# Kernel optimization log

Measured on AMD Instinct MI355X. Metric: run time of the kernel, lower is better.

The kernel has to match this reference:

```python
import jax, jax.numpy as jnp
import numpy as np

N_NODES = 50000
N_EDGES = 800000
IN_F, OUT_F = 128, 128
NUM_HEADS, QUERY_DIM = 3, 8


def setup_inputs() -> dict:
    key = jax.random.key(0)
    ks = jax.random.split(key, 8)
    scale = 1.0 / np.sqrt(IN_F)
    return {
        "x": jax.random.normal(ks[0], (N_NODES, IN_F), dtype=jnp.float32),
        "adj": jax.random.randint(ks[1], (2, N_EDGES), 0, N_NODES, dtype=jnp.int64),
        "Wq": jax.random.normal(ks[2], (QUERY_DIM * NUM_HEADS, IN_F), dtype=jnp.float32) * scale,
        "bq": jax.random.normal(ks[3], (QUERY_DIM * NUM_HEADS,), dtype=jnp.float32) * 0.01,
        "aw": jax.random.normal(ks[4], (NUM_HEADS, 2 * QUERY_DIM * NUM_HEADS), dtype=jnp.float32) * 0.1,
        "ab": jax.random.normal(ks[5], (NUM_HEADS,), dtype=jnp.float32) * 0.01,
        "lw": jax.random.normal(ks[6], (OUT_F, IN_F), dtype=jnp.float32) * scale,
        "lb": jax.random.normal(ks[7], (OUT_F,), dtype=jnp.float32) * 0.01,
    }


def reference(x, adj, Wq, bq, aw, ab, lw, lb):
    n = x.shape[0]
    s, r = adj[0], adj[1]
    # per-node query features: [N, H*Q]
    attr = x @ Wq.T + bq
    # per-edge attention logits from concat(sender, receiver): [E, H]
    e = jnp.concatenate((attr[s], attr[r]), axis=1) @ aw.T + ab
    # segment softmax over incoming edges of each receiver
    seg_max = jax.ops.segment_max(e, r, num_segments=n)  # [N, H]
    e = jnp.exp(e - jax.lax.stop_gradient(seg_max)[r])
    denom = jax.ops.segment_sum(e, r, num_segments=n)  # [N, H]
    alpha = e / jnp.maximum(denom[r], 1e-16)  # [E, H]
    # node value projection and attention-weighted aggregation
    h = x @ lw.T + lb  # [N, OUT_F]
    msg = h[s] * alpha.mean(axis=1, keepdims=True)  # [E, OUT_F]
    out = jax.ops.segment_sum(msg, r, num_segments=n)  # [N, OUT_F]
    return jax.nn.silu(out)
```

## Files before the change

kernel.cpp:

```cpp
#include <hip/hip_runtime.h>
#include <hip/hip_fp16.h>
#include <math.h>

#define N_NODES 50000
#define N_EDGES 800000
#define IN_F 128
#define OUT_F 128
#define NH 3
#define SCAN_NB ((N_NODES + 255) / 256)
#define NODE_NB ((N_NODES + 31) / 32)
#define NBH 32
#define EPB (N_EDGES / NBH)
#define QNODES (N_NODES / 4)
#define CQ_BLOCKS (NBH * 4)
#define NSLICE 4
#define SLICE_HALVES ((size_t)N_NODES * 32)

typedef __attribute__((ext_vector_type(8))) _Float16 f16x8;
typedef __attribute__((ext_vector_type(4))) float f32x4;
typedef __attribute__((ext_vector_type(2))) int i32x2;

__global__ __launch_bounds__(256) void weights_kernel(
    const float* __restrict__ Wq, const float* __restrict__ bq,
    const float* __restrict__ aw, const float* __restrict__ ab,
    const float* __restrict__ lw,
    _Float16* __restrict__ w2h, float* __restrict__ b2,
    _Float16* __restrict__ lwh)
{
    int t = blockIdx.x * 256 + threadIdx.x;
    if (t < 16 * 128) {
        int prow = t >> 7;
        int i    = t & 127;
        int r = -1;
        if (prow < 3) r = prow;
        else if (prow >= 4 && prow < 7) r = prow - 1;
        if (r < 0) {
            w2h[prow * 128 + i] = (_Float16)0.0f;
        } else {
            int hh  = (r < 3) ? r : r - 3;
            int off = (r < 3) ? 0 : 24;
            const float* awr = aw + hh * 48 + off;
            float acc = 0.0f;
            #pragma unroll
            for (int q = 0; q < 24; q++) acc += awr[q] * Wq[q * 128 + i];
            w2h[prow * 128 + i] = (_Float16)acc;
            if (i == 0) {
                float b = 0.0f;
                #pragma unroll
                for (int q = 0; q < 24; q++) b += awr[q] * bq[q];
                if (r >= 3) b += ab[hh];
                b2[r] = b;
            }
        }
    }
    int u = t - 16 * 128;
    if (u >= 0 && u < 128 * 128) lwh[u] = (_Float16)lw[u];
}

__global__ __launch_bounds__(256) void node_count_kernel(
    const float* __restrict__ x, const _Float16* __restrict__ lwh,
    const float* __restrict__ lb, const _Float16* __restrict__ w2h,
    const float* __restrict__ b2, const int* __restrict__ adj,
    __half* __restrict__ h, float* __restrict__ as4, float* __restrict__ ar4,
    unsigned int* __restrict__ hist, unsigned short* __restrict__ rank)
{
    __shared__ __align__(16) unsigned int shmem[QNODES / 2];

    if (blockIdx.x < CQ_BLOCKS) {
        unsigned int* cnt = shmem;
        for (int i = threadIdx.x; i < QNODES / 2; i += 256) cnt[i] = 0;
        __syncthreads();
        const int c = blockIdx.x >> 2, q = blockIdx.x & 3;
        const int nlo = q * QNODES;
        const int e0 = c * EPB, e1 = e0 + EPB;
        for (int base = e0 + threadIdx.x; base < e1; base += 8 * 256) {
            int rs[8];
            #pragma unroll
            for (int u = 0; u < 8; u++) {
                int e = base + u * 256;
                rs[u] = (e < e1) ? adj[N_EDGES + e] : -1;
            }
            #pragma unroll
            for (int u = 0; u < 8; u++) {
                int e = base + u * 256;
                int lr = rs[u] - nlo;
                if ((unsigned)lr < (unsigned)QNODES) {
                    int sh = (lr & 1) * 16;
                    unsigned int old = atomicAdd(&cnt[lr >> 1], 1u << sh);
                    rank[e] = (unsigned short)(old >> sh);
                }
            }
        }
        __syncthreads();
        unsigned int* hb = hist + (size_t)c * (N_NODES / 2) + q * (QNODES / 2);
        for (int i = threadIdx.x; i < QNODES / 2; i += 256)
            hb[i] = cnt[i];
        return;
    }

    unsigned char* xs = (unsigned char*)shmem;
    const int tx = threadIdx.x;
    const int nb = (blockIdx.x - CQ_BLOCKS) * 32;

    #pragma unroll
    for (int it = 0; it < 2; it++) {
        int cc = it * 256 + tx;
        int node = cc >> 4, kc = cc & 15;
        int gn = nb + node;
        f16x8 v;
        if (gn < N_NODES) {
            const float4* xr = (const float4*)(x + (size_t)gn * 128 + kc * 8);
            float4 p = xr[0], qq = xr[1];
            v[0] = (_Float16)p.x;  v[1] = (_Float16)p.y;
            v[2] = (_Float16)p.z;  v[3] = (_Float16)p.w;
            v[4] = (_Float16)qq.x; v[5] = (_Float16)qq.y;
            v[6] = (_Float16)qq.z; v[7] = (_Float16)qq.w;
        } else {
            #pragma unroll
            for (int e = 0; e < 8; e++) v[e] = (_Float16)0.0f;
        }
        int byte = node * 256 + ((kc * 16) ^ ((node & 7) << 4));
        *(f16x8*)(xs + byte) = v;
    }
    __syncthreads();

    const int wave = tx >> 6, lane = tx & 63;
    const int l15 = lane & 15, lg = lane >> 4;

    f16x8 afr[2][4];
    #pragma unroll
    for (int m = 0; m < 2; m++) {
        int out = wave * 32 + m * 16 + l15;
        const f16x8* ar8 = (const f16x8*)(lwh + (size_t)out * 128);
        #pragma unroll
        for (int kk = 0; kk < 4; kk++)
            afr[m][kk] = ar8[kk * 4 + lg];
    }
    f16x8 a6[4];
    {
        const f16x8* w8 = (const f16x8*)(w2h + (size_t)l15 * 128);
        #pragma unroll
        for (int kk = 0; kk < 4; kk++) a6[kk] = w8[kk * 4 + lg];
    }

    f32x4 acc[2][2], acc6[2];
    #pragma unroll
    for (int m = 0; m < 2; m++)
        #pragma unroll
        for (int n = 0; n < 2; n++)
            acc[m][n] = (f32x4){0.f, 0.f, 0.f, 0.f};
    #pragma unroll
    for (int n = 0; n < 2; n++) acc6[n] = (f32x4){0.f, 0.f, 0.f, 0.f};

    #pragma unroll
    for (int kk = 0; kk < 4; kk++) {
        f16x8 bfr[2];
        #pragma unroll
        for (int n = 0; n < 2; n++) {
            int node = n * 16 + l15;
            int byte = node * 256 + ((kk * 64 + lg * 16) ^ ((node & 7) << 4));
            bfr[n] = *(const f16x8*)(xs + byte);
        }
        #pragma unroll
        for (int m = 0; m < 2; m++)
            #pragma unroll
            for (int n = 0; n < 2; n++)
                acc[m][n] = __builtin_amdgcn_mfma_f32_16x16x32_f16(
                    afr[m][kk], bfr[n], acc[m][n], 0, 0, 0);
        if (wave == 0) {
            #pragma unroll
            for (int n = 0; n < 2; n++)
                acc6[n] = __builtin_amdgcn_mfma_f32_16x16x32_f16(
                    a6[kk], bfr[n], acc6[n], 0, 0, 0);
        }
    }

    #pragma unroll
    for (int n = 0; n < 2; n++) {
        int gn = nb + n * 16 + l15;
        if (gn >= N_NODES) continue;
        #pragma unroll
        for (int m = 0; m < 2; m++) {
            int outb = wave * 32 + m * 16 + lg * 4;
            float4 lbv = *(const float4*)&lb[outb];
            __half2 p0 = __floats2half2_rn(acc[m][n].x + lbv.x, acc[m][n].y + lbv.y);
            __half2 p1 = __floats2half2_rn(acc[m][n].z + lbv.z, acc[m][n].w + lbv.w);
            int2 st;
            st.x = *(int*)&p0;
            st.y = *(int*)&p1;
            *(int2*)&h[(size_t)wave * SLICE_HALVES + (size_t)gn * 32 + (outb & 31)] = st;
        }
    }

    if (wave == 0 && lg < 2) {
        float b0, bx, by;
        if (lg == 0) { b0 = b2[0]; bx = b2[1]; by = b2[2]; }
        else         { b0 = b2[3]; bx = b2[4]; by = b2[5]; }
        #pragma unroll
        for (int n = 0; n < 2; n++) {
            int gn = nb + n * 16 + l15;
            if (gn >= N_NODES) continue;
            float4 v = make_float4(acc6[n].x + b0, acc6[n].y + bx,
                                   acc6[n].z + by, 0.0f);
            if (lg == 0) *(float4*)&as4[(size_t)gn * 4] = v;
            else         *(float4*)&ar4[(size_t)gn * 4] = v;
        }
    }
}

__global__ __launch_bounds__(256) void scan_kernel(
    const unsigned int* __restrict__ hist, int* __restrict__ start,
    unsigned short* __restrict__ offs16,
    int* __restrict__ psum, int* __restrict__ poffs, int* __restrict__ sync)
{
    const int t = threadIdx.x, b = blockIdx.x;
    const int i = b * 256 + t;
    const int w = i >> 1, sh = (i & 1) * 16;
    int tot = 0;
    if (i < N_NODES) {
        for (int c = 0; c < NBH; c++)
            tot += (hist[(size_t)c * (N_NODES / 2) + w] >> sh) & 0xffff;
    }
    __shared__ int shm[256];
    shm[t] = tot;
    __syncthreads();
    #pragma unroll
    for (int off = 1; off < 256; off <<= 1) {
        int u = (t >= off) ? shm[t - off] : 0;
        __syncthreads();
        shm[t] += u;
        __syncthreads();
    }
    const int incl = shm[t];
    if (t == 255)
        __hip_atomic_store(&psum[b], incl, __ATOMIC_RELAXED,
                           __HIP_MEMORY_SCOPE_AGENT);
    __syncthreads();
    if (t == 0)
        __hip_atomic_fetch_add(&sync[0], 1, __ATOMIC_RELEASE,
                               __HIP_MEMORY_SCOPE_AGENT);

    if (b == 0) {
        if (t == 0)
            while (__hip_atomic_load(&sync[0], __ATOMIC_ACQUIRE,
                                     __HIP_MEMORY_SCOPE_AGENT) < SCAN_NB) {}
        __syncthreads();
        int pv = (t < SCAN_NB)
               ? __hip_atomic_load(&psum[t], __ATOMIC_RELAXED,
                                   __HIP_MEMORY_SCOPE_AGENT)
               : 0;
        shm[t] = pv;
        __syncthreads();
        #pragma unroll
        for (int off = 1; off < 256; off <<= 1) {
            int u = (t >= off) ? shm[t - off] : 0;
            __syncthreads();
            shm[t] += u;
            __syncthreads();
        }
        if (t < SCAN_NB)
            __hip_atomic_store(&poffs[t], shm[t] - pv, __ATOMIC_RELAXED,
                               __HIP_MEMORY_SCOPE_AGENT);
        __syncthreads();
        if (t == 0)
            __hip_atomic_store(&sync[1], 1, __ATOMIC_RELEASE,
                               __HIP_MEMORY_SCOPE_AGENT);
    }

    if (t == 0)
        while (__hip_atomic_load(&sync[1], __ATOMIC_ACQUIRE,
                                 __HIP_MEMORY_SCOPE_AGENT) == 0) {}
    __syncthreads();
    const int base = __hip_atomic_load(&poffs[b], __ATOMIC_RELAXED,
                                       __HIP_MEMORY_SCOPE_AGENT);
    if (i < N_NODES) {
        start[i] = base + incl - tot;
        int acc = 0;
        for (int c = 0; c < NBH; c++) {
            offs16[(size_t)c * N_NODES + i] = (unsigned short)acc;
            acc += (hist[(size_t)c * (N_NODES / 2) + w] >> sh) & 0xffff;
        }
    }
    if (i == N_NODES - 1) start[N_NODES] = base + incl;
}

__global__ __launch_bounds__(256) void fill_kernel(
    const int* __restrict__ adj, const int* __restrict__ start,
    const unsigned short* __restrict__ offs16,
    const unsigned short* __restrict__ rank,
    unsigned short* __restrict__ srcs)
{
    int e = blockIdx.x * 512 + threadIdx.x;
    #pragma unroll
    for (int u = 0; u < 2; u++, e += 256) {
        if (e < N_EDGES) {
            int r = adj[N_EDGES + e];
            int cb = e / EPB;
            int pos = start[r] + (int)offs16[(size_t)cb * N_NODES + r]
                    + (int)rank[e];
            srcs[pos] = (unsigned short)adj[e];
        }
    }
}

__global__ __launch_bounds__(256) void coef_kernel(
    const int* __restrict__ start, const unsigned short* __restrict__ srcs,
    const float4* __restrict__ as4, const float* __restrict__ ar4,
    i32x2* __restrict__ ec)
{
    const int wave = threadIdx.x >> 6;
    const int lane = threadIdx.x & 63;
    const int n = blockIdx.x * 4 + wave;
    if (n >= N_NODES) return;
    const int s0 = start[n], s1 = start[n + 1];
    const int deg = s1 - s0;
    const float4 cr = *(const float4*)&ar4[(size_t)n * 4];

    if (deg <= 64) {
        float e0 = 0.f, e1 = 0.f, e2 = 0.f;
        int s = 0;
        if (lane < deg) {
            s = srcs[s0 + lane];
            float4 a = as4[s];
            e0 = __expf(a.x + cr.x);
            e1 = __expf(a.y + cr.y);
            e2 = __expf(a.z + cr.z);
        }
        float p0 = e0, p1 = e1, p2 = e2;
        #pragma unroll
        for (int off = 32; off >= 1; off >>= 1) {
            p0 += __shfl_xor(p0, off);
            p1 += __shfl_xor(p1, off);
            p2 += __shfl_xor(p2, off);
        }
        const float i0 = (1.0f / 3.0f) / fmaxf(p0, 1e-30f);
        const float i1 = (1.0f / 3.0f) / fmaxf(p1, 1e-30f);
        const float i2 = (1.0f / 3.0f) / fmaxf(p2, 1e-30f);
        if (lane < deg) {
            i32x2 v;
            v.x = s;
            v.y = __float_as_int(e0 * i0 + e1 * i1 + e2 * i2);
            ec[s0 + lane] = v;
        }
    } else {
        float p0 = 0.f, p1 = 0.f, p2 = 0.f;
        for (int k = s0 + lane; k < s1; k += 64) {
            float4 a = as4[srcs[k]];
            p0 += __expf(a.x + cr.x);
            p1 += __expf(a.y + cr.y);
            p2 += __expf(a.z + cr.z);
        }
        #pragma unroll
        for (int off = 32; off >= 1; off >>= 1) {
            p0 += __shfl_xor(p0, off);
            p1 += __shfl_xor(p1, off);
            p2 += __shfl_xor(p2, off);
        }
        const float i0 = (1.0f / 3.0f) / fmaxf(p0, 1e-30f);
        const float i1 = (1.0f / 3.0f) / fmaxf(p1, 1e-30f);
        const float i2 = (1.0f / 3.0f) / fmaxf(p2, 1e-30f);
        for (int k = s0 + lane; k < s1; k += 64) {
            int s = srcs[k];
            float4 a = as4[s];
            i32x2 v;
            v.x = s;
            v.y = __float_as_int(__expf(a.x + cr.x) * i0
                               + __expf(a.y + cr.y) * i1
                               + __expf(a.z + cr.z) * i2);
            ec[k] = v;
        }
    }
}

__global__ __launch_bounds__(256) void spmm_kernel(
    const int* __restrict__ start, const i32x2* __restrict__ ec,
    const __half* __restrict__ h, float* __restrict__ out)
{
    const int slice = blockIdx.x & 3;
    const int tile  = blockIdx.x >> 2;
    const int wave  = threadIdx.x >> 6;
    const int lane  = threadIdx.x & 63;
    const int grp   = lane >> 4;
    const int gl    = lane & 15;
    const int jo    = gl >> 2;
    const int cpart = gl & 3;
    const int n = tile * 16 + wave * 4 + grp;

    const int4* hsl = (const int4*)(h + (size_t)slice * SLICE_HALVES);

    float a0 = 0.f, a1 = 0.f, a2 = 0.f, a3 = 0.f;
    float a4 = 0.f, a5 = 0.f, a6 = 0.f, a7 = 0.f;

    if (n < N_NODES) {
        const int s0 = start[n], s1 = start[n + 1];
        #pragma unroll 2
        for (int k = s0 + jo; k < s1; k += 4) {
            i32x2 E = ec[k];
            int4 hv = hsl[(size_t)(unsigned)E.x * 4 + cpart];
            float c = __int_as_float(E.y);
            float2 f0 = __half22float2(*(const __half2*)&hv.x);
            float2 f1 = __half22float2(*(const __half2*)&hv.y);
            float2 f2 = __half22float2(*(const __half2*)&hv.z);
            float2 f3 = __half22float2(*(const __half2*)&hv.w);
            a0 = fmaf(f0.x, c, a0); a1 = fmaf(f0.y, c, a1);
            a2 = fmaf(f1.x, c, a2); a3 = fmaf(f1.y, c, a3);
            a4 = fmaf(f2.x, c, a4); a5 = fmaf(f2.y, c, a5);
            a6 = fmaf(f3.x, c, a6); a7 = fmaf(f3.y, c, a7);
        }
    }

    a0 += __shfl_xor(a0, 4); a0 += __shfl_xor(a0, 8);
    a1 += __shfl_xor(a1, 4); a1 += __shfl_xor(a1, 8);
    a2 += __shfl_xor(a2, 4); a2 += __shfl_xor(a2, 8);
    a3 += __shfl_xor(a3, 4); a3 += __shfl_xor(a3, 8);
    a4 += __shfl_xor(a4, 4); a4 += __shfl_xor(a4, 8);
    a5 += __shfl_xor(a5, 4); a5 += __shfl_xor(a5, 8);
    a6 += __shfl_xor(a6, 4); a6 += __shfl_xor(a6, 8);
    a7 += __shfl_xor(a7, 4); a7 += __shfl_xor(a7, 8);

    if (jo == 0 && n < N_NODES) {
        float4 o0, o1;
        o0.x = a0 / (1.0f + __expf(-a0));
        o0.y = a1 / (1.0f + __expf(-a1));
        o0.z = a2 / (1.0f + __expf(-a2));
        o0.w = a3 / (1.0f + __expf(-a3));
        o1.x = a4 / (1.0f + __expf(-a4));
        o1.y = a5 / (1.0f + __expf(-a5));
        o1.z = a6 / (1.0f + __expf(-a6));
        o1.w = a7 / (1.0f + __expf(-a7));
        float* op = out + (size_t)n * 128 + slice * 32 + cpart * 8;
        *(float4*)op = o0;
        *(float4*)(op + 4) = o1;
    }
}

extern "C" void kernel_launch(void* const* d_in, const int* in_sizes, int n_in,
                              void* d_out, int out_size, void* d_ws, size_t ws_size,
                              hipStream_t stream)
{
    const float* x  = (const float*)d_in[0];
    const int*   adj= (const int*)  d_in[1];
    const float* Wq = (const float*)d_in[2];
    const float* bq = (const float*)d_in[3];
    const float* aw = (const float*)d_in[4];
    const float* ab = (const float*)d_in[5];
    const float* lw = (const float*)d_in[6];
    const float* lb = (const float*)d_in[7];
    float* out = (float*)d_out;

    _Float16* w2h = (_Float16*)d_ws;
    float* b2     = (float*)(w2h + 2048);
    _Float16* lwh = (_Float16*)(b2 + 8);
    float* as4    = (float*)(lwh + 16384);
    float* ar4    = as4 + (size_t)N_NODES * 4;
    __half* h     = (__half*)(ar4 + (size_t)N_NODES * 4);
    i32x2* ec     = (i32x2*)(h + (size_t)N_NODES * 128);
    int* start    = (int*)(ec + N_EDGES);
    int* sync     = start + (N_NODES + 1);
    unsigned int* hist = (unsigned int*)(sync + 8);
    unsigned short* offs16 = (unsigned short*)(hist + (size_t)NBH * (N_NODES / 2));
    unsigned short* rank   = offs16 + (size_t)NBH * N_NODES;
    unsigned short* srcs   = rank + N_EDGES;
    int* psum     = (int*)(srcs + N_EDGES);
    int* poffs    = psum + 256;

    hipMemsetAsync(sync, 0, 8 * sizeof(int), stream);

    weights_kernel<<<72, 256, 0, stream>>>(Wq, bq, aw, ab, lw, w2h, b2, lwh);

    node_count_kernel<<<CQ_BLOCKS + NODE_NB, 256, 0, stream>>>(
        x, lwh, lb, w2h, b2, adj, h, as4, ar4, hist, rank);

    scan_kernel<<<SCAN_NB, 256, 0, stream>>>(hist, start, offs16,
                                             psum, poffs, sync);

    fill_kernel<<<(N_EDGES + 511) / 512, 256, 0, stream>>>(
        adj, start, offs16, rank, srcs);

    coef_kernel<<<(N_NODES + 3) / 4, 256, 0, stream>>>(
        start, srcs, (const float4*)as4, ar4, ec);

    spmm_kernel<<<NSLICE * (N_NODES / 16), 256, 0, stream>>>(
        start, ec, h, out);
}
```

Baseline: 129.5 us.

## Make SpMM persistent with XCC-affine slice scheduling and atomic tile tickets

Turns the SpMM into a persistent kernel of 2048 blocks. Each block reads its XCC id from a hardware register, starts on a matching feature slice so that slice's fp16 rows stay in that die's L2, and takes 64-node tiles from an atomic ticket counter. Each node is now handled by 4 lanes that walk all its edges in sequence, which removes the cross-lane shuffle reduction. The fp16 convert plus FMA is replaced by inline v_fma_mix_f32. The costs are two block syncs per tile, longer serial loops per lane, and dependence on counters that the existing memset zeroes.

```diff
diff --git a/kernel.cpp b/kernel.cpp
--- a/kernel.cpp
+++ b/kernel.cpp
@@ -15,10 +15,19 @@
 #define CQ_BLOCKS (NBH * 4)
 #define NSLICE 4
 #define SLICE_HALVES ((size_t)N_NODES * 32)
+#define TILES_PER_SLICE ((N_NODES + 63) / 64)
+#define HWREG(id, off, sz) ((((sz)-1) << 11) | ((off) << 6) | (id))
 
 typedef __attribute__((ext_vector_type(8))) _Float16 f16x8;
 typedef __attribute__((ext_vector_type(4))) float f32x4;
 typedef __attribute__((ext_vector_type(2))) int i32x2;
+
+#define FMA_MIX_LO(acc, w, c) \
+    asm("v_fma_mix_f32 %0, %1, %2, %0 op_sel:[0,0,0] op_sel_hi:[1,0,0]" \
+        : "+v"(acc) : "v"(w), "v"(c))
+#define FMA_MIX_HI(acc, w, c) \
+    asm("v_fma_mix_f32 %0, %1, %2, %0 op_sel:[1,0,0] op_sel_hi:[1,0,0]" \
+        : "+v"(acc) : "v"(w), "v"(c))
 
 __global__ __launch_bounds__(256) void weights_kernel(
     const float* __restrict__ Wq, const float* __restrict__ bq,
@@ -374,63 +383,60 @@
 
 __global__ __launch_bounds__(256) void spmm_kernel(
     const int* __restrict__ start, const i32x2* __restrict__ ec,
-    const __half* __restrict__ h, float* __restrict__ out)
-{
-    const int slice = blockIdx.x & 3;
-    const int tile  = blockIdx.x >> 2;
-    const int wave  = threadIdx.x >> 6;
-    const int lane  = threadIdx.x & 63;
-    const int grp   = lane >> 4;
-    const int gl    = lane & 15;
-    const int jo    = gl >> 2;
-    const int cpart = gl & 3;
-    const int n = tile * 16 + wave * 4 + grp;
-
-    const int4* hsl = (const int4*)(h + (size_t)slice * SLICE_HALVES);
-
-    float a0 = 0.f, a1 = 0.f, a2 = 0.f, a3 = 0.f;
-    float a4 = 0.f, a5 = 0.f, a6 = 0.f, a7 = 0.f;
-
-    if (n < N_NODES) {
-        const int s0 = start[n], s1 = start[n + 1];
-        #pragma unroll 2
-        for (int k = s0 + jo; k < s1; k += 4) {
-            i32x2 E = ec[k];
-            int4 hv = hsl[(size_t)(unsigned)E.x * 4 + cpart];
-            float c = __int_as_float(E.y);
-            float2 f0 = __half22float2(*(const __half2*)&hv.x);
-            float2 f1 = __half22float2(*(const __half2*)&hv.y);
-            float2 f2 = __half22float2(*(const __half2*)&hv.z);
-            float2 f3 = __half22float2(*(const __half2*)&hv.w);
-            a0 = fmaf(f0.x, c, a0); a1 = fmaf(f0.y, c, a1);
-            a2 = fmaf(f1.x, c, a2); a3 = fmaf(f1.y, c, a3);
-            a4 = fmaf(f2.x, c, a4); a5 = fmaf(f2.y, c, a5);
-            a6 = fmaf(f3.x, c, a6); a7 = fmaf(f3.y, c, a7);
-        }
-    }
-
-    a0 += __shfl_xor(a0, 4); a0 += __shfl_xor(a0, 8);
-    a1 += __shfl_xor(a1, 4); a1 += __shfl_xor(a1, 8);
-    a2 += __shfl_xor(a2, 4); a2 += __shfl_xor(a2, 8);
-    a3 += __shfl_xor(a3, 4); a3 += __shfl_xor(a3, 8);
-    a4 += __shfl_xor(a4, 4); a4 += __shfl_xor(a4, 8);
-    a5 += __shfl_xor(a5, 4); a5 += __shfl_xor(a5, 8);
-    a6 += __shfl_xor(a6, 4); a6 += __shfl_xor(a6, 8);
-    a7 += __shfl_xor(a7, 4); a7 += __shfl_xor(a7, 8);
-
-    if (jo == 0 && n < N_NODES) {
-        float4 o0, o1;
-        o0.x = a0 / (1.0f + __expf(-a0));
-        o0.y = a1 / (1.0f + __expf(-a1));
-        o0.z = a2 / (1.0f + __expf(-a2));
-        o0.w = a3 / (1.0f + __expf(-a3));
-        o1.x = a4 / (1.0f + __expf(-a4));
-        o1.y = a5 / (1.0f + __expf(-a5));
-        o1.z = a6 / (1.0f + __expf(-a6));
-        o1.w = a7 / (1.0f + __expf(-a7));
-        float* op = out + (size_t)n * 128 + slice * 32 + cpart * 8;
-        *(float4*)op = o0;
-        *(float4*)(op + 4) = o1;
+    const __half* __restrict__ h, int* __restrict__ ticket,
+    float* __restrict__ out)
+{
+    const int wave = threadIdx.x >> 6;
+    const int lane = threadIdx.x & 63;
+    const int quad = lane >> 2;
+    const int cpart = lane & 3;
+
+    __shared__ int s_tile;
+    const int xcc = (int)__builtin_amdgcn_s_getreg(HWREG(20, 0, 8));
+
+    for (int t = 0; t < NSLICE; ++t) {
+        const int sl = (xcc + t) & 3;
+        const int4* hp = (const int4*)(h + (size_t)sl * SLICE_HALVES);
+        while (true) {
+            if (threadIdx.x == 0)
+                s_tile = atomicAdd(&ticket[sl], 1);
+            __syncthreads();
+            const int tile = s_tile;
+            __syncthreads();
+            if (tile >= TILES_PER_SLICE) break;
+
+            const int n = tile * 64 + wave * 16 + quad;
+            int s0 = 0, s1 = 0;
+            if (n < N_NODES) { s0 = start[n]; s1 = start[n + 1]; }
+
+            float a0 = 0.f, a1 = 0.f, a2 = 0.f, a3 = 0.f;
+            float a4 = 0.f, a5 = 0.f, a6 = 0.f, a7 = 0.f;
+            #pragma unroll 4
+            for (int k = s0; k < s1; ++k) {
+                i32x2 E = ec[k];
+                int4 hv = hp[(size_t)(unsigned)E.x * 4 + cpart];
+                float c = __int_as_float(E.y);
+                FMA_MIX_LO(a0, hv.x, c); FMA_MIX_HI(a1, hv.x, c);
+                FMA_MIX_LO(a2, hv.y, c); FMA_MIX_HI(a3, hv.y, c);
+                FMA_MIX_LO(a4, hv.z, c); FMA_MIX_HI(a5, hv.z, c);
+                FMA_MIX_LO(a6, hv.w, c); FMA_MIX_HI(a7, hv.w, c);
+            }
+
+            if (n < N_NODES) {
+                float4 o0, o1;
+                o0.x = a0 / (1.0f + __expf(-a0));
+                o0.y = a1 / (1.0f + __expf(-a1));
+                o0.z = a2 / (1.0f + __expf(-a2));
+                o0.w = a3 / (1.0f + __expf(-a3));
+                o1.x = a4 / (1.0f + __expf(-a4));
+                o1.y = a5 / (1.0f + __expf(-a5));
+                o1.z = a6 / (1.0f + __expf(-a6));
+                o1.w = a7 / (1.0f + __expf(-a7));
+                float* op = out + (size_t)n * 128 + sl * 32 + cpart * 8;
+                *(float4*)op = o0;
+                *(float4*)(op + 4) = o1;
+            }
+        }
     }
 }
 
@@ -480,6 +486,6 @@
     coef_kernel<<<(N_NODES + 3) / 4, 256, 0, stream>>>(
         start, srcs, (const float4*)as4, ar4, ec);
 
-    spmm_kernel<<<NSLICE * (N_NODES / 16), 256, 0, stream>>>(
-        start, ec, h, out);
-}
+    spmm_kernel<<<2048, 256, 0, stream>>>(
+        start, ec, h, sync + 4, out);
+}
```

Result: slower. 221.4 us (+71.0%).
